# Kernel tuning notes

Measured on AMD Instinct MI355X. Metric: run time of the kernel, lower is better.

The kernel has to match this reference:

```python
import jax, jax.numpy as jnp
import numpy as np
from math import sqrt

DIM = 2048
N_HEADS = 2
HEAD_DIM = DIM // N_HEADS  # 1024 == RoPE dims (dim // 2)
ROPE_DIMS = DIM // 2
ROPE_BASE = 10000.0


def apply_rope(x, dims=ROPE_DIMS, base=ROPE_BASE, offset=0):
    # x: [B, H, L, Dh]; non-traditional (split-half) RoPE over sequence axis
    L = x.shape[-2]
    pos = jnp.arange(offset, offset + L, dtype=x.dtype)[:, None]          # [L,1]
    inv = jnp.exp(jnp.arange(0, dims, 2, dtype=x.dtype) * (-np.log(base) / dims))  # [dims//2]
    theta = pos * inv                                                      # [L, dims//2]
    cos, sin = jnp.cos(theta), jnp.sin(theta)
    h = dims // 2
    x1, x2 = x[..., :h], x[..., h:dims]
    rx1 = x1 * cos - x2 * sin
    rx2 = x1 * sin + x2 * cos
    if dims < x.shape[-1]:
        return jnp.concatenate([rx1, rx2, x[..., dims:]], axis=-1)
    return jnp.concatenate([rx1, rx2], axis=-1)


def setup_inputs() -> dict:
    key = jax.random.key(0)
    ks = jax.random.split(key, 6)
    B, L = 4, 2048
    x = jax.random.normal(ks[0], (B, L, DIM), dtype=jnp.float32)
    # causal additive mask
    causal = jnp.tril(jnp.ones((L, L), dtype=bool))
    mask = jnp.where(causal, 0.0, -1e9).astype(jnp.float32)
    s1 = 1.0 / sqrt(DIM)
    Wqkv_w = jax.random.normal(ks[1], (3 * DIM, DIM), dtype=jnp.float32) * s1
    Wqkv_b = jnp.zeros((3 * DIM,), dtype=jnp.float32)
    out_w = jax.random.normal(ks[2], (DIM, DIM), dtype=jnp.float32) * s1
    out_b = jnp.zeros((DIM,), dtype=jnp.float32)
    return {"x": x, "mask": mask, "Wqkv_w": Wqkv_w, "Wqkv_b": Wqkv_b,
            "out_w": out_w, "out_b": out_b}


def reference(x, mask, Wqkv_w, Wqkv_b, out_w, out_b):
    B, L, D = x.shape
    H, Dh = N_HEADS, HEAD_DIM
    qkv = x @ Wqkv_w.T + Wqkv_b                       # [B, L, 3D]
    q, k, v = jnp.split(qkv, 3, axis=-1)
    # b l (h d) -> b h l d
    split = lambda t: t.reshape(B, L, H, Dh).transpose(0, 2, 1, 3)
    q, k, v = split(q), split(k), split(v)
    q = apply_rope(q)
    k = apply_rope(k)
    scale = sqrt(1.0 / Dh)
    scores = jnp.einsum('bhld,bhkd->bhlk', q * scale, k)  # [B,H,L,L]
    scores = scores + mask                                 # additive causal mask
    probs = jax.nn.softmax(scores, axis=-1)
    vh = jnp.einsum('bhlk,bhkd->bhld', probs, v)
    vh = vh.transpose(0, 2, 1, 3).reshape(B, L, D)         # b h l d -> b l (h d)
    out = vh @ out_w.T + out_b
    return (out, k, v)
```

## Files before the change

kernel.cpp:

```cpp
#include <hip/hip_runtime.h>
#include <hip/hip_bf16.h>
#include <math.h>

typedef unsigned short u16;
typedef __attribute__((ext_vector_type(8))) __bf16 bf16x8;
typedef __attribute__((ext_vector_type(4))) float f32x4;

__device__ __forceinline__ u16 f2b(float f) {
  unsigned u = __builtin_bit_cast(unsigned, f);
  u += 0x7fffu + ((u >> 16) & 1u);
  return (u16)(u >> 16);
}
__device__ __forceinline__ float b2f(u16 h) {
  unsigned u = ((unsigned)h) << 16;
  return __builtin_bit_cast(float, u);
}

__device__ __forceinline__ void gld_lds16(const u16* g, u16* l) {
  __builtin_amdgcn_global_load_lds(
      (const __attribute__((address_space(1))) unsigned int*)g,
      (__attribute__((address_space(3))) unsigned int*)l, 16, 0, 0);
}

template <class FA, class FB, class FC>
__device__ __forceinline__ void gemm128_body(FA fa, FB fb, FC fc, int m0,
                                             int n0, int K) {
  __shared__ __align__(16) u16 As[128 * 64];
  __shared__ __align__(16) u16 Bs[128 * 64];
  const int tid = threadIdx.x;
  const int wave = tid >> 6;
  const int lane = tid & 63;
  const int srow = lane >> 3;
  const int scol = ((lane & 7) ^ srow) * 8;
  const int wm = (wave & 1) * 64;
  const int wn = (wave >> 1) * 64;
  const int fm = lane & 15;
  const int fs = fm & 7;

  f32x4 acc[4][4];
#pragma unroll
  for (int i = 0; i < 4; ++i)
#pragma unroll
    for (int j = 0; j < 4; ++j) acc[i][j] = (f32x4){0.f, 0.f, 0.f, 0.f};

  for (int k0 = 0; k0 < K; k0 += 64) {
#pragma unroll
    for (int c = 0; c < 4; ++c) {
      int chunk = c * 4 + wave;
      int row = chunk * 8 + srow;
      gld_lds16(fa(m0 + row, k0 + scol), &As[chunk * 512]);
      gld_lds16(fb(n0 + row, k0 + scol), &Bs[chunk * 512]);
    }
    __syncthreads();
#pragma unroll
    for (int kk = 0; kk < 2; ++kk) {
      const int cb = kk * 4 + (lane >> 4);
      const int p8 = (cb ^ fs) * 8;
      bf16x8 af[4], bfr[4];
#pragma unroll
      for (int i = 0; i < 4; ++i)
        af[i] = *(const bf16x8*)&As[(wm + i * 16 + fm) * 64 + p8];
#pragma unroll
      for (int j = 0; j < 4; ++j)
        bfr[j] = *(const bf16x8*)&Bs[(wn + j * 16 + fm) * 64 + p8];
#pragma unroll
      for (int i = 0; i < 4; ++i)
#pragma unroll
        for (int j = 0; j < 4; ++j)
          acc[i][j] = __builtin_amdgcn_mfma_f32_16x16x32_bf16(
              af[i], bfr[j], acc[i][j], 0, 0, 0);
    }
    __syncthreads();
  }
  const int er = lane >> 4;
#pragma unroll
  for (int i = 0; i < 4; ++i)
#pragma unroll
    for (int j = 0; j < 4; ++j)
#pragma unroll
      for (int r = 0; r < 4; ++r) {
        int m = m0 + wm + i * 16 + er * 4 + r;
        int n = n0 + wn + j * 16 + fm;
        fc(m, n, acc[i][j][r]);
      }
}

struct FAB {
  const u16* p;
  int ld;
  __device__ __forceinline__ const u16* operator()(int r, int k) const {
    return p + (size_t)r * ld + k;
  }
};
struct FAvh {
  const u16* q;
  __device__ __forceinline__ const u16* operator()(int m, int k) const {
    int b = m >> 11, l = m & 2047, h = k >> 10, kk = k & 1023;
    return q + ((size_t)((b << 1) + h) * 2048 + l) * 1024 + kk;
  }
};
struct EQKV {
  u16* qb;
  u16* kb;
  float* vout;
  const float* bias;
  __device__ __forceinline__ void operator()(int m, int n, float v) const {
    v += bias[n];
    int b = m >> 11, l = m & 2047;
    int part = n >> 11, nn = n & 2047, h = nn >> 10, d = nn & 1023;
    size_t idx = ((size_t)((b << 1) + h) * 2048 + l) * 1024 + d;
    if (part == 0)
      qb[idx] = f2b(v);
    else if (part == 1)
      kb[idx] = f2b(v);
    else
      vout[idx] = v;
  }
};
struct EScore {
  float* S;
  __device__ __forceinline__ void operator()(int m, int n, float v) const {
    S[((size_t)m << 11) + n] = v * 0.03125f + (n > m ? -1.0e9f : 0.0f);
  }
};
struct EBf16 {
  u16* o;
  int ld;
  __device__ __forceinline__ void operator()(int m, int n, float v) const {
    o[(size_t)m * ld + n] = f2b(v);
  }
};
struct EOut {
  float* o;
  const float* bias;
  __device__ __forceinline__ void operator()(int m, int n, float v) const {
    o[((size_t)m << 11) + n] = v + bias[n];
  }
};

__global__ void __launch_bounds__(256) k_cast(const float* in, u16* out) {
  int i = (blockIdx.x * 256 + threadIdx.x) * 4;
  float4 f = *(const float4*)(in + i);
  ushort4 o;
  o.x = f2b(f.x);
  o.y = f2b(f.y);
  o.z = f2b(f.z);
  o.w = f2b(f.w);
  *(ushort4*)(out + i) = o;
}

__global__ void __launch_bounds__(256) k_qkv(const u16* xb, const u16* wb,
                                             const float* bias, u16* qb,
                                             u16* kb, float* vout) {
  gemm128_body(FAB{xb, 2048}, FAB{wb, 2048}, EQKV{qb, kb, vout, bias},
               blockIdx.y * 128, blockIdx.x * 128, 2048);
}

__global__ void __launch_bounds__(256) k_rope(u16* qb, u16* kb, float* kout) {
  int row = blockIdx.x;
  int l = row & 2047;
  size_t base = (size_t)row * 1024;
  float lf = (float)l;
  const float c0 = (float)(-9.210340371976184 / 1024.0);
  for (int i = threadIdx.x; i < 512; i += 256) {
    float inv = expf((float)(2 * i) * c0);
    float th = lf * inv;
    float c = cosf(th), s = sinf(th);
    float x1 = b2f(qb[base + i]), x2 = b2f(qb[base + 512 + i]);
    qb[base + i] = f2b(x1 * c - x2 * s);
    qb[base + 512 + i] = f2b(x1 * s + x2 * c);
    float y1 = b2f(kb[base + i]), y2 = b2f(kb[base + 512 + i]);
    float r1 = y1 * c - y2 * s, r2 = y1 * s + y2 * c;
    kb[base + i] = f2b(r1);
    kb[base + 512 + i] = f2b(r2);
    kout[base + i] = r1;
    kout[base + 512 + i] = r2;
  }
}

__global__ void __launch_bounds__(256) k_transpose_v(const float* v, u16* vt) {
  __shared__ u16 tile[64][65];
  int bh = blockIdx.z;
  int d0 = blockIdx.x * 64, l0 = blockIdx.y * 64;
  const float* vb = v + (size_t)bh * 2048 * 1024;
  u16* vtb = vt + (size_t)bh * 1024 * 2048;
  int t = threadIdx.x;
  int c = t & 63, r4 = t >> 6;
#pragma unroll
  for (int r = 0; r < 16; ++r) {
    int row = r * 4 + r4;
    tile[row][c] = f2b(vb[(size_t)(l0 + row) * 1024 + d0 + c]);
  }
  __syncthreads();
#pragma unroll
  for (int r = 0; r < 16; ++r) {
    int drow = r * 4 + r4;
    vtb[(size_t)(d0 + drow) * 2048 + l0 + c] = tile[c][drow];
  }
}

__global__ void __launch_bounds__(256) k_score(const u16* qb, const u16* kb,
                                               float* S, int zbase) {
  int m0 = blockIdx.y * 128, n0 = blockIdx.x * 128;
  if (n0 > m0) return;
  int z = blockIdx.z, bh = zbase + z;
  const u16* q = qb + (size_t)bh * 2048 * 1024;
  const u16* k = kb + (size_t)bh * 2048 * 1024;
  float* Sz = S + (size_t)z * 2048 * 2048;
  gemm128_body(FAB{q, 1024}, FAB{k, 1024}, EScore{Sz}, m0, n0, 1024);
}

__global__ void __launch_bounds__(256) k_softmax(const float* S, u16* P) {
  int l = blockIdx.x, z = blockIdx.y;
  const float* Srow = S + ((size_t)z * 2048 + l) * 2048;
  u16* Prow = P + ((size_t)z * 2048 + l) * 2048;
  int t = threadIdx.x;
  int jend = ((l >> 7) + 1) << 7;
  __shared__ float red[4];
  float vals[8];
  float mx = -1e30f;
#pragma unroll
  for (int i = 0; i < 8; ++i) {
    int j = i * 256 + t;
    float v = (j <= l) ? Srow[j] : -1e30f;
    vals[i] = v;
    mx = fmaxf(mx, v);
  }
#pragma unroll
  for (int off = 32; off; off >>= 1) mx = fmaxf(mx, __shfl_down(mx, off));
  if ((t & 63) == 0) red[t >> 6] = mx;
  __syncthreads();
  mx = fmaxf(fmaxf(red[0], red[1]), fmaxf(red[2], red[3]));
  __syncthreads();
  float sum = 0.f;
#pragma unroll
  for (int i = 0; i < 8; ++i) {
    int j = i * 256 + t;
    float e = (j <= l) ? __expf(vals[i] - mx) : 0.f;
    vals[i] = e;
    sum += e;
  }
#pragma unroll
  for (int off = 32; off; off >>= 1) sum += __shfl_down(sum, off);
  if ((t & 63) == 0) red[t >> 6] = sum;
  __syncthreads();
  sum = red[0] + red[1] + red[2] + red[3];
  float is = 1.0f / sum;
#pragma unroll
  for (int i = 0; i < 8; ++i) {
    int j = i * 256 + t;
    if (j < jend) Prow[j] = f2b(vals[i] * is);
  }
}

__global__ void __launch_bounds__(256) k_pv(const u16* P, const u16* vt,
                                            u16* vh, int zbase) {
  int z = blockIdx.z, bh = zbase + z;
  int m0 = blockIdx.y * 128, n0 = blockIdx.x * 128;
  const u16* Pz = P + (size_t)z * 2048 * 2048;
  const u16* vtb = vt + (size_t)bh * 1024 * 2048;
  u16* outb = vh + (size_t)bh * 2048 * 1024;
  int Keff = m0 + 128;
  gemm128_body(FAB{Pz, 2048}, FAB{vtb, 2048}, EBf16{outb, 1024}, m0, n0, Keff);
}

__global__ void __launch_bounds__(256) k_out(const u16* vh, const u16* w2,
                                             const float* bias, float* out) {
  gemm128_body(FAvh{vh}, FAB{w2, 2048}, EOut{out, bias}, blockIdx.y * 128,
               blockIdx.x * 128, 2048);
}

extern "C" void kernel_launch(void* const* d_in, const int* in_sizes, int n_in,
                              void* d_out, int out_size, void* d_ws,
                              size_t ws_size, hipStream_t stream) {
  const float* x = (const float*)d_in[0];
  const float* w1 = (const float*)d_in[2];
  const float* b1 = (const float*)d_in[3];
  const float* w2 = (const float*)d_in[4];
  const float* b2 = (const float*)d_in[5];
  float* out = (float*)d_out;
  float* kout = out + (size_t)16777216;
  float* vout = kout + (size_t)16777216;

  char* ws = (char*)d_ws;
  u16* xb = (u16*)ws;
  ws += (size_t)33554432;
  u16* w1b = (u16*)ws;
  ws += (size_t)25165824;
  u16* w2b = (u16*)ws;
  ws += (size_t)8388608;
  u16* qb = (u16*)ws;
  ws += (size_t)33554432;
  u16* kb = (u16*)ws;
  ws += (size_t)33554432;
  u16* vtb = (u16*)ws;
  ws += (size_t)33554432;
  size_t used = (size_t)(ws - (char*)d_ws);
  size_t rem = ws_size > used ? ws_size - used : 0;
  size_t perz = (size_t)2048 * 2048 * 4 + (size_t)2048 * 2048 * 2;
  int Z = 1;
  if (rem >= 8 * perz)
    Z = 8;
  else if (rem >= 4 * perz)
    Z = 4;
  else if (rem >= 2 * perz)
    Z = 2;
  float* S = (float*)ws;
  u16* P = (u16*)(ws + (size_t)Z * 2048 * 2048 * 4);

  k_cast<<<16384, 256, 0, stream>>>(x, xb);
  k_cast<<<12288, 256, 0, stream>>>(w1, w1b);
  k_cast<<<4096, 256, 0, stream>>>(w2, w2b);
  k_qkv<<<dim3(48, 64), 256, 0, stream>>>(xb, w1b, b1, qb, kb, vout);
  k_rope<<<16384, 256, 0, stream>>>(qb, kb, kout);
  k_transpose_v<<<dim3(16, 32, 8), 256, 0, stream>>>(vout, vtb);
  for (int zb = 0; zb < 8; zb += Z) {
    k_score<<<dim3(16, 16, Z), 256, 0, stream>>>(qb, kb, S, zb);
    k_softmax<<<dim3(2048, Z), 256, 0, stream>>>(S, P);
    k_pv<<<dim3(8, 16, Z), 256, 0, stream>>>(P, vtb, qb, zb);
  }
  k_out<<<dim3(16, 64), 256, 0, stream>>>(qb, w2b, b2, out);
}
```

Before: 897.0 us.

## Simplify GEMM addressing, merge cast kernels, reuse RoPE trig, write PV output directly

The GEMM body now takes plain base pointers and leading dimensions with per-lane offsets computed once, replacing the functor address computation in the load loop. The three cast launches become one kernel. RoPE computes sin/cos once per position with fast intrinsics and reuses them across all eight batch-heads. PV writes its output in [B, L, H*Dh] layout to a new workspace buffer so the output GEMM reads it contiguously. This uses extra workspace, which can lower the softmax batching factor Z, and the fast intrinsics lose some trig accuracy.

```diff
diff --git a/kernel.cpp b/kernel.cpp
--- a/kernel.cpp
+++ b/kernel.cpp
@@ -22,9 +22,10 @@
       (__attribute__((address_space(3))) unsigned int*)l, 16, 0, 0);
 }
 
-template <class FA, class FB, class FC>
-__device__ __forceinline__ void gemm128_body(FA fa, FB fb, FC fc, int m0,
-                                             int n0, int K) {
+template <class FC>
+__device__ __forceinline__ void gemm128_body(const u16* A, int lda,
+                                             const u16* B, int ldb, FC fc,
+                                             int m0, int n0, int K) {
   __shared__ __align__(16) u16 As[128 * 64];
   __shared__ __align__(16) u16 Bs[128 * 64];
   const int tid = threadIdx.x;
@@ -37,6 +38,11 @@
   const int fm = lane & 15;
   const int fs = fm & 7;
 
+  const u16* Abase = A + (size_t)m0 * lda;
+  const u16* Bbase = B + (size_t)n0 * ldb;
+  const size_t aLane = (size_t)(wave * 8 + srow) * lda + scol;
+  const size_t bLane = (size_t)(wave * 8 + srow) * ldb + scol;
+
   f32x4 acc[4][4];
 #pragma unroll
   for (int i = 0; i < 4; ++i)
@@ -46,10 +52,10 @@
   for (int k0 = 0; k0 < K; k0 += 64) {
 #pragma unroll
     for (int c = 0; c < 4; ++c) {
-      int chunk = c * 4 + wave;
-      int row = chunk * 8 + srow;
-      gld_lds16(fa(m0 + row, k0 + scol), &As[chunk * 512]);
-      gld_lds16(fb(n0 + row, k0 + scol), &Bs[chunk * 512]);
+      gld_lds16(Abase + (aLane + (size_t)(c * 32) * lda + k0),
+                &As[(c * 4 + wave) * 512]);
+      gld_lds16(Bbase + (bLane + (size_t)(c * 32) * ldb + k0),
+                &Bs[(c * 4 + wave) * 512]);
     }
     __syncthreads();
 #pragma unroll
@@ -85,20 +91,6 @@
       }
 }
 
-struct FAB {
-  const u16* p;
-  int ld;
-  __device__ __forceinline__ const u16* operator()(int r, int k) const {
-    return p + (size_t)r * ld + k;
-  }
-};
-struct FAvh {
-  const u16* q;
-  __device__ __forceinline__ const u16* operator()(int m, int k) const {
-    int b = m >> 11, l = m & 2047, h = k >> 10, kk = k & 1023;
-    return q + ((size_t)((b << 1) + h) * 2048 + l) * 1024 + kk;
-  }
-};
 struct EQKV {
   u16* qb;
   u16* kb;
@@ -138,43 +130,66 @@
   }
 };
 
-__global__ void __launch_bounds__(256) k_cast(const float* in, u16* out) {
-  int i = (blockIdx.x * 256 + threadIdx.x) * 4;
-  float4 f = *(const float4*)(in + i);
+__global__ void __launch_bounds__(256) k_cast3(const float* x, const float* w1,
+                                               const float* w2, u16* xb,
+                                               u16* w1b, u16* w2b) {
+  long i = (long)(blockIdx.x * 256 + threadIdx.x) * 4;
+  const float* src;
+  u16* dst;
+  long off;
+  if (i < 16777216L) {
+    src = x; dst = xb; off = i;
+  } else if (i < 16777216L + 12582912L) {
+    src = w1; dst = w1b; off = i - 16777216L;
+  } else {
+    src = w2; dst = w2b; off = i - 16777216L - 12582912L;
+  }
+  float4 f = *(const float4*)(src + off);
   ushort4 o;
   o.x = f2b(f.x);
   o.y = f2b(f.y);
   o.z = f2b(f.z);
   o.w = f2b(f.w);
-  *(ushort4*)(out + i) = o;
+  *(ushort4*)(dst + off) = o;
 }
 
 __global__ void __launch_bounds__(256) k_qkv(const u16* xb, const u16* wb,
                                              const float* bias, u16* qb,
                                              u16* kb, float* vout) {
-  gemm128_body(FAB{xb, 2048}, FAB{wb, 2048}, EQKV{qb, kb, vout, bias},
-               blockIdx.y * 128, blockIdx.x * 128, 2048);
+  gemm128_body(xb, 2048, wb, 2048, EQKV{qb, kb, vout, bias}, blockIdx.y * 128,
+               blockIdx.x * 128, 2048);
 }
 
 __global__ void __launch_bounds__(256) k_rope(u16* qb, u16* kb, float* kout) {
-  int row = blockIdx.x;
-  int l = row & 2047;
-  size_t base = (size_t)row * 1024;
+  int l = blockIdx.x;
+  int t = threadIdx.x;
   float lf = (float)l;
   const float c0 = (float)(-9.210340371976184 / 1024.0);
-  for (int i = threadIdx.x; i < 512; i += 256) {
-    float inv = expf((float)(2 * i) * c0);
-    float th = lf * inv;
-    float c = cosf(th), s = sinf(th);
-    float x1 = b2f(qb[base + i]), x2 = b2f(qb[base + 512 + i]);
-    qb[base + i] = f2b(x1 * c - x2 * s);
-    qb[base + 512 + i] = f2b(x1 * s + x2 * c);
-    float y1 = b2f(kb[base + i]), y2 = b2f(kb[base + 512 + i]);
-    float r1 = y1 * c - y2 * s, r2 = y1 * s + y2 * c;
-    kb[base + i] = f2b(r1);
-    kb[base + 512 + i] = f2b(r2);
-    kout[base + i] = r1;
-    kout[base + 512 + i] = r2;
+  float s0, c_0, s1, c_1;
+  {
+    float inv = __expf((float)(2 * t) * c0);
+    __sincosf(lf * inv, &s0, &c_0);
+    float inv2 = __expf((float)(2 * (t + 256)) * c0);
+    __sincosf(lf * inv2, &s1, &c_1);
+  }
+#pragma unroll
+  for (int bh = 0; bh < 8; ++bh) {
+    size_t base = ((size_t)bh * 2048 + l) * 1024;
+#pragma unroll
+    for (int half = 0; half < 2; ++half) {
+      int i = t + half * 256;
+      float c = half ? c_1 : c_0;
+      float s = half ? s1 : s0;
+      float x1 = b2f(qb[base + i]), x2 = b2f(qb[base + 512 + i]);
+      qb[base + i] = f2b(x1 * c - x2 * s);
+      qb[base + 512 + i] = f2b(x1 * s + x2 * c);
+      float y1 = b2f(kb[base + i]), y2 = b2f(kb[base + 512 + i]);
+      float r1 = y1 * c - y2 * s, r2 = y1 * s + y2 * c;
+      kb[base + i] = f2b(r1);
+      kb[base + 512 + i] = f2b(r2);
+      kout[base + i] = r1;
+      kout[base + 512 + i] = r2;
+    }
   }
 }
 
@@ -207,7 +222,7 @@
   const u16* q = qb + (size_t)bh * 2048 * 1024;
   const u16* k = kb + (size_t)bh * 2048 * 1024;
   float* Sz = S + (size_t)z * 2048 * 2048;
-  gemm128_body(FAB{q, 1024}, FAB{k, 1024}, EScore{Sz}, m0, n0, 1024);
+  gemm128_body(q, 1024, k, 1024, EScore{Sz}, m0, n0, 1024);
 }
 
 __global__ void __launch_bounds__(256) k_softmax(const float* S, u16* P) {
@@ -256,17 +271,18 @@
 __global__ void __launch_bounds__(256) k_pv(const u16* P, const u16* vt,
                                             u16* vh, int zbase) {
   int z = blockIdx.z, bh = zbase + z;
+  int b = bh >> 1, h = bh & 1;
   int m0 = blockIdx.y * 128, n0 = blockIdx.x * 128;
   const u16* Pz = P + (size_t)z * 2048 * 2048;
   const u16* vtb = vt + (size_t)bh * 1024 * 2048;
-  u16* outb = vh + (size_t)bh * 2048 * 1024;
+  u16* outb = vh + (size_t)b * 2048 * 2048 + (size_t)h * 1024;
   int Keff = m0 + 128;
-  gemm128_body(FAB{Pz, 2048}, FAB{vtb, 2048}, EBf16{outb, 1024}, m0, n0, Keff);
+  gemm128_body(Pz, 2048, vtb, 2048, EBf16{outb, 2048}, m0, n0, Keff);
 }
 
 __global__ void __launch_bounds__(256) k_out(const u16* vh, const u16* w2,
                                              const float* bias, float* out) {
-  gemm128_body(FAvh{vh}, FAB{w2, 2048}, EOut{out, bias}, blockIdx.y * 128,
+  gemm128_body(vh, 2048, w2, 2048, EOut{out, bias}, blockIdx.y * 128,
                blockIdx.x * 128, 2048);
 }
 
@@ -294,6 +310,8 @@
   u16* kb = (u16*)ws;
   ws += (size_t)33554432;
   u16* vtb = (u16*)ws;
+  ws += (size_t)33554432;
+  u16* vh = (u16*)ws;
   ws += (size_t)33554432;
   size_t used = (size_t)(ws - (char*)d_ws);
   size_t rem = ws_size > used ? ws_size - used : 0;
@@ -308,16 +326,14 @@
   float* S = (float*)ws;
   u16* P = (u16*)(ws + (size_t)Z * 2048 * 2048 * 4);
 
-  k_cast<<<16384, 256, 0, stream>>>(x, xb);
-  k_cast<<<12288, 256, 0, stream>>>(w1, w1b);
-  k_cast<<<4096, 256, 0, stream>>>(w2, w2b);
+  k_cast3<<<32768, 256, 0, stream>>>(x, w1, w2, xb, w1b, w2b);
   k_qkv<<<dim3(48, 64), 256, 0, stream>>>(xb, w1b, b1, qb, kb, vout);
-  k_rope<<<16384, 256, 0, stream>>>(qb, kb, kout);
+  k_rope<<<2048, 256, 0, stream>>>(qb, kb, kout);
   k_transpose_v<<<dim3(16, 32, 8), 256, 0, stream>>>(vout, vtb);
   for (int zb = 0; zb < 8; zb += Z) {
     k_score<<<dim3(16, 16, Z), 256, 0, stream>>>(qb, kb, S, zb);
     k_softmax<<<dim3(2048, Z), 256, 0, stream>>>(S, P);
-    k_pv<<<dim3(8, 16, Z), 256, 0, stream>>>(P, vtb, qb, zb);
-  }
-  k_out<<<dim3(16, 64), 256, 0, stream>>>(qb, w2b, b2, out);
-}
+    k_pv<<<dim3(8, 16, Z), 256, 0, stream>>>(P, vtb, vh, zb);
+  }
+  k_out<<<dim3(16, 64), 256, 0, stream>>>(vh, w2b, b2, out);
+}
```

Result: faster. 877.6 us (-2.2%).
